# Kernel optimization log

Hardware: AMD Instinct MI355X
Metric: run time of the kernel (lower is better)

The kernel has to match this reference:

```python
import jax, jax.numpy as jnp
import numpy as np

B, S, D = 2, 2048, 1024
FFN = 4096
E, TOPK = 4, 2
H, WIN = 8, 128
EPS = 1e-6


def rmsnorm(x, w):
    rms = jax.lax.rsqrt(jnp.mean(x * x, axis=-1, keepdims=True) + EPS)
    return x * rms * w


def linear_scan(x, a):
    """h_t = a_t * h_{t-1} + x_t along axis=1, via associative scan."""
    def comb(c1, c2):
        a1, x1 = c1
        a2, x2 = c2
        return (a1 * a2, a2 * x1 + x2)
    _, h = jax.lax.associative_scan(comb, (a, x), axis=1)
    return h


def mingru_expert(xn, Wg, bg, Wv, bv, Wd, bd):
    g = xn @ Wg + bg
    v = xn @ Wv + bv
    d = xn @ Wd + bd
    x_scan = jax.nn.sigmoid(g) * jnp.tanh(v)
    a = 0.001 + 0.998 * jax.nn.sigmoid(d)
    return linear_scan(x_scan, a)


def setup_inputs() -> dict:
    key = jax.random.key(0)
    ks = jax.random.split(key, 16)
    sc = 0.02
    return {
        "x": jax.random.normal(ks[0], (B, S, D), jnp.float32),
        "rms_mix_w": jnp.ones((D,), jnp.float32),
        "gate_w": jax.random.normal(ks[1], (D, E), jnp.float32) * sc,
        "Wg": jax.random.normal(ks[2], (E, D, D), jnp.float32) * sc,
        "bg": jnp.zeros((E, D), jnp.float32),
        "Wv": jax.random.normal(ks[3], (E, D, D), jnp.float32) * sc,
        "bv": jnp.zeros((E, D), jnp.float32),
        "Wd": jax.random.normal(ks[4], (E, D, D), jnp.float32) * sc,
        "bd": jnp.ones((E, D), jnp.float32),  # decay_bias_init = 1.0
        "rms_attn_w": jnp.ones((D,), jnp.float32),
        "w_qkv": jax.random.normal(ks[5], (D, 3 * D), jnp.float32) * sc,
        "w_attn_out": jax.random.normal(ks[6], (D, D), jnp.float32) * sc,
        "rms_ffn_w": jnp.ones((D,), jnp.float32),
        "w_ffn_gate": jax.random.normal(ks[7], (D, FFN), jnp.float32) * sc,
        "w_ffn_up": jax.random.normal(ks[8], (D, FFN), jnp.float32) * sc,
        "w_ffn_out": jax.random.normal(ks[9], (FFN, D), jnp.float32) * sc,
    }


def reference(x, rms_mix_w, gate_w, Wg, bg, Wv, bv, Wd, bd,
              rms_attn_w, w_qkv, w_attn_out,
              rms_ffn_w, w_ffn_gate, w_ffn_up, w_ffn_out):
    # --- MoE-MinGRU mixer -------------------------------------------------
    xn = rmsnorm(x, rms_mix_w)
    gate_logits = xn @ gate_w                         # [B,S,E]
    top_vals, top_idx = jax.lax.top_k(gate_logits, TOPK)
    weights = jax.nn.softmax(top_vals, axis=-1)       # [B,S,K]
    expert_outs = jax.vmap(mingru_expert, in_axes=(None, 0, 0, 0, 0, 0, 0))(
        xn, Wg, bg, Wv, bv, Wd, bd)                   # [E,B,S,D]
    expert_outs = jnp.moveaxis(expert_outs, 0, 2)     # [B,S,E,D]
    gathered = jnp.take_along_axis(expert_outs, top_idx[..., None], axis=2)  # [B,S,K,D]
    mix = jnp.sum(weights[..., None] * gathered, axis=2)
    x = x + mix

    # --- Sliding-window causal attention ----------------------------------
    xn = rmsnorm(x, rms_attn_w)
    dh = D // H
    qkv = (xn @ w_qkv).reshape(B, S, 3, H, dh)
    q, k, v = qkv[:, :, 0], qkv[:, :, 1], qkv[:, :, 2]  # [B,S,H,dh]
    scores = jnp.einsum("bqhd,bkhd->bhqk", q, k) / jnp.sqrt(jnp.float32(dh))
    i = jnp.arange(S)[:, None]
    j = jnp.arange(S)[None, :]
    allowed = (j <= i) & (j > i - WIN)
    scores = jnp.where(allowed, scores, -jnp.inf)
    attn = jax.nn.softmax(scores, axis=-1)
    ao = jnp.einsum("bhqk,bkhd->bqhd", attn, v).reshape(B, S, D)
    x = x + ao @ w_attn_out

    # --- SwiGLU FFN --------------------------------------------------------
    xn = rmsnorm(x, rms_ffn_w)
    ffn = (jax.nn.silu(xn @ w_ffn_gate) * (xn @ w_ffn_up)) @ w_ffn_out
    return x + ffn
```

## Files before the change

kernel.cpp:

```cpp
#include <hip/hip_runtime.h>
#include <hip/hip_bf16.h>
#include <math.h>

constexpr int kB   = 2;
constexpr int kS   = 2048;
constexpr int kD   = 1024;
constexpr int kFFN = 4096;
constexpr int kM   = kB * kS;
constexpr int kH   = 8;
constexpr int kDH  = 128;
constexpr int kNC  = 64;
constexpr int kT   = kS / kNC;
constexpr int kNE  = 12288;

typedef unsigned short u16;
typedef __attribute__((ext_vector_type(8))) short short8;
typedef __attribute__((ext_vector_type(4))) float f32x4;

__device__ __forceinline__ float sigf(float x) { return 1.0f / (1.0f + __expf(-x)); }
__device__ __forceinline__ float bu2f(u16 u) { return __uint_as_float(((unsigned)u) << 16); }
__device__ __forceinline__ u16 f2bu(float f) {
    __hip_bfloat16 h = __float2bfloat16(f);
    return reinterpret_cast<u16&>(h);
}
__device__ __forceinline__ void async16(const void* g, void* l) {
    __builtin_amdgcn_global_load_lds((const __attribute__((address_space(1))) void*)g,
                                     (__attribute__((address_space(3))) void*)l, 16, 0, 0);
}
__device__ __forceinline__ int xcd_swz(int orig, int nwg) {
    const int xcd = orig & 7;
    const int q8 = nwg >> 3, r8 = nwg & 7;
    return (xcd < r8 ? xcd * (q8 + 1) : r8 * (q8 + 1) + (xcd - r8) * q8) + (orig >> 3);
}

__global__ __launch_bounds__(256) void rmsnorm_k(const float* __restrict__ x,
                                                 const float* __restrict__ w,
                                                 u16* __restrict__ o)
{
    __shared__ float red[4];
    const int row = blockIdx.x;
    const int t = threadIdx.x;
    float4 v = ((const float4*)(x + (size_t)row * kD))[t];
    float ss = v.x*v.x + v.y*v.y + v.z*v.z + v.w*v.w;
    #pragma unroll
    for (int m = 32; m; m >>= 1) ss += __shfl_xor(ss, m);
    if ((t & 63) == 0) red[t >> 6] = ss;
    __syncthreads();
    float tot = red[0] + red[1] + red[2] + red[3];
    float r = rsqrtf(tot * (1.0f / (float)kD) + 1e-6f);
    float4 wv = ((const float4*)w)[t];
    ushort4 u;
    u.x = f2bu(v.x * r * wv.x); u.y = f2bu(v.y * r * wv.y);
    u.z = f2bu(v.z * r * wv.z); u.w = f2bu(v.w * r * wv.w);
    ((ushort4*)(o + (size_t)row * kD))[t] = u;
}

__global__ __launch_bounds__(64) void routing_k(const float* __restrict__ x,
                                                const float* __restrict__ wmix,
                                                const float* __restrict__ gw,
                                                float* __restrict__ wts,
                                                int* __restrict__ idx)
{
    const int row = blockIdx.x;
    const int lane = threadIdx.x;
    const float* xr = x + (size_t)row * kD;
    float ss = 0.0f;
    for (int d = lane; d < kD; d += 64) { float v = xr[d]; ss = fmaf(v, v, ss); }
    #pragma unroll
    for (int m = 32; m; m >>= 1) ss += __shfl_xor(ss, m);
    float r = rsqrtf(ss * (1.0f / (float)kD) + 1e-6f);

    float a0 = 0, a1 = 0, a2 = 0, a3 = 0;
    for (int d = lane; d < kD; d += 64) {
        float xv = xr[d] * wmix[d];
        float4 g = ((const float4*)gw)[d];
        a0 = fmaf(xv, g.x, a0);
        a1 = fmaf(xv, g.y, a1);
        a2 = fmaf(xv, g.z, a2);
        a3 = fmaf(xv, g.w, a3);
    }
    #pragma unroll
    for (int m = 32; m; m >>= 1) {
        a0 += __shfl_xor(a0, m);
        a1 += __shfl_xor(a1, m);
        a2 += __shfl_xor(a2, m);
        a3 += __shfl_xor(a3, m);
    }
    if (lane == 0) {
        float a[4] = {a0, a1, a2, a3};
        int i0 = 0; float v0 = a[0];
        #pragma unroll
        for (int e = 1; e < 4; ++e) if (a[e] > v0) { v0 = a[e]; i0 = e; }
        int i1 = -1; float v1 = -INFINITY;
        #pragma unroll
        for (int e = 0; e < 4; ++e) if (e != i0 && a[e] > v1) { v1 = a[e]; i1 = e; }
        float e1 = __expf(r * (v1 - v0));
        float dn = 1.0f + e1;
        wts[row * 2 + 0] = 1.0f / dn;
        wts[row * 2 + 1] = e1 / dn;
        idx[row * 2 + 0] = i0;
        idx[row * 2 + 1] = i1;
    }
}

__global__ __launch_bounds__(256) void transp_k(const float* __restrict__ src,
                                                u16* __restrict__ dst,
                                                int rows, int cols,
                                                size_t sstride, size_t dstride)
{
    __shared__ float t[32][33];
    const float* s = src + blockIdx.z * sstride;
    u16* d = dst + blockIdx.z * dstride;
    const int c0 = blockIdx.x * 32, r0 = blockIdx.y * 32;
    const int tc = threadIdx.x & 31, tr4 = (threadIdx.x >> 5) * 4;
    #pragma unroll
    for (int i = 0; i < 4; ++i)
        t[tr4 + i][tc] = s[(size_t)(r0 + tr4 + i) * cols + c0 + tc];
    __syncthreads();
    #pragma unroll
    for (int i = 0; i < 4; ++i) {
        int cc = tr4 + i;
        d[(size_t)(c0 + cc) * rows + r0 + tc] = f2bu(t[tc][cc]);
    }
}

__global__ __launch_bounds__(256) void biaspack_k(const float* __restrict__ bg,
                                                  const float* __restrict__ bv,
                                                  const float* __restrict__ bd,
                                                  float* __restrict__ pb)
{
    int e = blockIdx.y;
    int r = blockIdx.x * 256 + threadIdx.x;
    const float* src = (r < 1024) ? bg : (r < 2048) ? bv : bd;
    pb[e * 3072 + r] = src[e * 1024 + (r & 1023)];
}

template<bool BIAS, bool SILU, bool MUL, bool NT>
__global__ __launch_bounds__(512, 2) void gemmA_k(
    const u16* __restrict__ A, const u16* __restrict__ BT,
    const float* __restrict__ bias, const u16* __restrict__ mulsrc,
    u16* __restrict__ Cout, int N, int K)
{
    __shared__ __align__(16) u16 lds[2][32768];
    const int tid = threadIdx.x;
    const int l = tid & 63;
    const int w = tid >> 6;
    const int wr = w >> 2, wc = w & 3;
    const int fr = l & 15, g = l >> 4;

    const int gx = gridDim.x;
    const int wg = xcd_swz(blockIdx.y * gx + blockIdx.x, gx * gridDim.y);
    const int bm = (wg / gx) * 256, bn = (wg % gx) * 256;

    const int srow = l >> 3;
    const int scol = (l & 7) ^ srow;
    const u16* gA = A  + (size_t)(bm + srow) * K + scol * 8;
    const u16* gB = BT + (size_t)(bn + srow) * K + scol * 8;

    auto STAGE = [&](int kt, int sb) {
        u16* dst = lds[sb] + l * 8;
        const int k0 = kt * 64;
        #pragma unroll
        for (int i = 0; i < 4; ++i) {
            int chunk = w * 4 + i;
            async16(gA + (size_t)chunk * 8 * K + k0, dst + chunk * 512);
            async16(gB + (size_t)chunk * 8 * K + k0, dst + 16384 + chunk * 512);
        }
    };

    f32x4 acc[8][4];
    #pragma unroll
    for (int m = 0; m < 8; ++m)
        #pragma unroll
        for (int n = 0; n < 4; ++n) acc[m][n] = (f32x4){0.f, 0.f, 0.f, 0.f};

    STAGE(0, 0);
    __syncthreads();
    const int nt = K >> 6;
    for (int t = 0; t < nt; ++t) {
        const int cb = t & 1;
        if (t + 1 < nt) STAGE(t + 1, cb ^ 1);
        const u16* bA = lds[cb];
        const u16* bB = lds[cb] + 16384;
        #pragma unroll
        for (int ks = 0; ks < 2; ++ks) {
            const int xo = ((ks * 4 + g) ^ (fr & 7)) * 8;
            short8 b[4];
            #pragma unroll
            for (int n = 0; n < 4; ++n)
                b[n] = *(const short8*)(bB + (wc * 64 + n * 16 + fr) * 64 + xo);
            #pragma unroll
            for (int m = 0; m < 8; ++m) {
                short8 a = *(const short8*)(bA + (wr * 128 + m * 16 + fr) * 64 + xo);
                #pragma unroll
                for (int n = 0; n < 4; ++n)
                    acc[m][n] = __builtin_amdgcn_mfma_f32_16x16x32_bf16(a, b[n], acc[m][n], 0, 0, 0);
            }
        }
        __syncthreads();
    }

    const int orow0 = bm + wr * 128 + g * 4;
    const int ocol0 = bn + wc * 64 + fr;
    float bi[4];
    if constexpr (BIAS) {
        #pragma unroll
        for (int n = 0; n < 4; ++n) bi[n] = bias[ocol0 + n * 16];
    }
    #pragma unroll
    for (int m = 0; m < 8; ++m) {
        #pragma unroll
        for (int r = 0; r < 4; ++r) {
            const size_t ro = (size_t)(orow0 + m * 16 + r) * N;
            #pragma unroll
            for (int n = 0; n < 4; ++n) {
                const size_t off = ro + ocol0 + n * 16;
                float v = acc[m][n][r];
                if constexpr (BIAS) v += bi[n];
                if constexpr (SILU) v = v * sigf(v);
                if constexpr (MUL)  v *= bu2f(mulsrc[off]);
                if constexpr (NT) __builtin_nontemporal_store((short)f2bu(v), (short*)(Cout + off));
                else              Cout[off] = f2bu(v);
            }
        }
    }
}

__global__ __launch_bounds__(512, 2) void gemmO_k(
    const u16* __restrict__ A, const u16* __restrict__ BT,
    const float* __restrict__ res, float* __restrict__ Cout,
    int N, int K)
{
    __shared__ __align__(16) u16 lds[2][20480];
    const int tid = threadIdx.x;
    const int l = tid & 63;
    const int w = tid >> 6;
    const int wr = w >> 1, wc = w & 1;
    const int fr = l & 15, g = l >> 4;

    const int gx = gridDim.x;
    const int wg = xcd_swz(blockIdx.y * gx + blockIdx.x, gx * gridDim.y);
    const int bm = (wg / gx) * 256, bn = (wg % gx) * 64;

    const int srow = l >> 3;
    const int scol = (l & 7) ^ srow;
    const u16* gA = A  + (size_t)(bm + srow) * K + scol * 8;
    const u16* gB = BT + (size_t)(bn + srow) * K + scol * 8;

    auto STAGE = [&](int kt, int sb) {
        u16* dst = lds[sb] + l * 8;
        const int k0 = kt * 64;
        #pragma unroll
        for (int i = 0; i < 4; ++i) {
            int chunk = w * 4 + i;
            async16(gA + (size_t)chunk * 8 * K + k0, dst + chunk * 512);
        }
        async16(gB + (size_t)w * 8 * K + k0, dst + 16384 + w * 512);
    };

    f32x4 acc[4][2];
    #pragma unroll
    for (int m = 0; m < 4; ++m)
        #pragma unroll
        for (int n = 0; n < 2; ++n) acc[m][n] = (f32x4){0.f, 0.f, 0.f, 0.f};

    STAGE(0, 0);
    __syncthreads();
    const int nt = K >> 6;
    for (int t = 0; t < nt; ++t) {
        const int cb = t & 1;
        if (t + 1 < nt) STAGE(t + 1, cb ^ 1);
        const u16* bA = lds[cb];
        const u16* bB = lds[cb] + 16384;
        #pragma unroll
        for (int ks = 0; ks < 2; ++ks) {
            const int xo = ((ks * 4 + g) ^ (fr & 7)) * 8;
            short8 a[4], b[2];
            #pragma unroll
            for (int m = 0; m < 4; ++m)
                a[m] = *(const short8*)(bA + (wr * 64 + m * 16 + fr) * 64 + xo);
            #pragma unroll
            for (int n = 0; n < 2; ++n)
                b[n] = *(const short8*)(bB + (wc * 32 + n * 16 + fr) * 64 + xo);
            #pragma unroll
            for (int m = 0; m < 4; ++m)
                #pragma unroll
                for (int n = 0; n < 2; ++n)
                    acc[m][n] = __builtin_amdgcn_mfma_f32_16x16x32_bf16(a[m], b[n], acc[m][n], 0, 0, 0);
        }
        __syncthreads();
    }

    const int orow0 = bm + wr * 64 + g * 4;
    const int ocol0 = bn + wc * 32 + fr;
    #pragma unroll
    for (int m = 0; m < 4; ++m) {
        #pragma unroll
        for (int r = 0; r < 4; ++r) {
            const size_t ro = (size_t)(orow0 + m * 16 + r) * N;
            #pragma unroll
            for (int n = 0; n < 2; ++n) {
                const size_t off = ro + ocol0 + n * 16;
                Cout[off] = acc[m][n][r] + res[off];
            }
        }
    }
}

__global__ __launch_bounds__(256) void scan1_k(const u16* __restrict__ gvdall,
                                               float* __restrict__ sumA,
                                               float* __restrict__ sumX)
{
    const int e = blockIdx.y;
    int i = blockIdx.x * 256 + threadIdx.x;
    int d = i & (kD - 1);
    int c = (i >> 10) & (kNC - 1);
    int b = i >> 16;
    const u16* gvd = gvdall + e * 3072;
    size_t base = ((size_t)b * kS + c * kT) * kNE + d;
    float A = 1.0f, X = 0.0f;
    for (int t = 0; t < kT; ++t) {
        size_t ix = base + (size_t)t * kNE;
        float xs = sigf(bu2f(gvd[ix])) * tanhf(bu2f(gvd[ix + 1024]));
        float a  = 0.001f + 0.998f * sigf(bu2f(gvd[ix + 2048]));
        A *= a;
        X = fmaf(a, X, xs);
    }
    size_t si = ((size_t)(e * kNC + c) * kB + b) * kD + d;
    sumA[si] = A;
    sumX[si] = X;
}

__global__ __launch_bounds__(256) void scan2_k(const float* __restrict__ sumA,
                                               const float* __restrict__ sumX,
                                               float* __restrict__ carry)
{
    const int e = blockIdx.y;
    int bd = blockIdx.x * 256 + threadIdx.x;
    float h = 0.0f;
    for (int c = 0; c < kNC; ++c) {
        size_t si = ((size_t)(e * kNC + c)) * (kB * kD) + bd;
        carry[si] = h;
        h = fmaf(sumA[si], h, sumX[si]);
    }
}

__global__ __launch_bounds__(256) void scan3_k(const u16* __restrict__ gvdall,
                                               const float* __restrict__ carry,
                                               const int* __restrict__ tidx,
                                               u16* __restrict__ slot0,
                                               u16* __restrict__ slot1)
{
    const int e = blockIdx.y;
    int i = blockIdx.x * 256 + threadIdx.x;
    int d = i & (kD - 1);
    int c = (i >> 10) & (kNC - 1);
    int b = i >> 16;
    const u16* gvd = gvdall + e * 3072;
    size_t base = ((size_t)b * kS + c * kT) * kNE + d;
    float h = carry[((size_t)(e * kNC + c) * kB + b) * kD + d];
    const int tok0 = b * kS + c * kT;
    for (int t = 0; t < kT; ++t) {
        size_t ix = base + (size_t)t * kNE;
        float xs = sigf(bu2f(gvd[ix])) * tanhf(bu2f(gvd[ix + 1024]));
        float a  = 0.001f + 0.998f * sigf(bu2f(gvd[ix + 2048]));
        h = fmaf(a, h, xs);
        const int tok = tok0 + t;
        const size_t o = (size_t)tok * kD + d;
        if (e == tidx[tok * 2])          slot0[o] = f2bu(h);
        else if (e == tidx[tok * 2 + 1]) slot1[o] = f2bu(h);
    }
}

__global__ __launch_bounds__(256) void mix_k(const float* __restrict__ x,
                                             const u16* __restrict__ slot0,
                                             const u16* __restrict__ slot1,
                                             const float* __restrict__ wts,
                                             float* __restrict__ xo)
{
    size_t i = (size_t)blockIdx.x * 256 + threadIdx.x;
    int m = (int)(i >> 8);
    float w0 = wts[m * 2 + 0], w1 = wts[m * 2 + 1];
    float4 xv = ((const float4*)x)[i];
    ushort4 h0 = ((const ushort4*)slot0)[i];
    ushort4 h1 = ((const ushort4*)slot1)[i];
    float4 o;
    o.x = xv.x + w0 * bu2f(h0.x) + w1 * bu2f(h1.x);
    o.y = xv.y + w0 * bu2f(h0.y) + w1 * bu2f(h1.y);
    o.z = xv.z + w0 * bu2f(h0.z) + w1 * bu2f(h1.z);
    o.w = xv.w + w0 * bu2f(h0.w) + w1 * bu2f(h1.w);
    ((float4*)xo)[i] = o;
}

__global__ __launch_bounds__(256) void transpV_k(const u16* __restrict__ qkvb,
                                                 u16* __restrict__ vT)
{
    __shared__ u16 t[64][68];
    const int tid = threadIdx.x;
    const int s0 = blockIdx.x * 64;
    const int d0 = blockIdx.y * 64;
    const int bh = blockIdx.z;
    const int bb = bh >> 3, hh = bh & 7;
    const u16* src = qkvb + (size_t)(bb * kS + s0) * 3072 + 2048 + hh * kDH + d0;
    for (int idx = tid; idx < 64 * 16; idx += 256) {
        int sl = idx >> 4, c4 = (idx & 15) * 4;
        *(ushort4*)&t[sl][c4] = *(const ushort4*)(src + (size_t)sl * 3072 + c4);
    }
    __syncthreads();
    u16* dst = vT + ((size_t)bh * kDH + d0) * kS + s0;
    for (int idx = tid; idx < 64 * 16; idx += 256) {
        int dl = idx >> 4, s4 = (idx & 15) * 4;
        ushort4 v;
        v.x = t[s4 + 0][dl]; v.y = t[s4 + 1][dl];
        v.z = t[s4 + 2][dl]; v.w = t[s4 + 3][dl];
        *(ushort4*)(dst + (size_t)dl * kS + s4) = v;
    }
}

__global__ __launch_bounds__(256) void attn_mfma_k(const u16* __restrict__ qkvb,
                                                   const u16* __restrict__ vT,
                                                   u16* __restrict__ aob)
{
    __shared__ __align__(16) u16 KV[26112];
    __shared__ __align__(16) u16 P[4 * 16 * 200];

    const int tid = threadIdx.x;
    const int lane = tid & 63;
    const int w = tid >> 6;
    const int fr = lane & 15, g = lane >> 4;
    const int q0 = blockIdx.x * 64;
    const int hh = blockIdx.y;
    const int bb = blockIdx.z;
    const int kbase = q0 - 128;
    const float scale = 0.08838834764831845f;

    const u16* qkv_b = qkvb + (size_t)bb * kS * 3072 + hh * kDH;

    for (int idx = tid; idx < 192 * 16; idx += 256) {
        int k = idx >> 4, c = idx & 15;
        int kg = kbase + k; if (kg < 0) kg = 0;
        short8 v = *(const short8*)(qkv_b + (size_t)kg * 3072 + 1024 + c * 8);
        *(short8*)(&KV[k * 136 + c * 8]) = v;
    }
    short8 qf[4];
    {
        const u16* qrow = qkv_b + (size_t)(q0 + w * 16 + fr) * 3072 + g * 8;
        #pragma unroll
        for (int s = 0; s < 4; ++s) qf[s] = *(const short8*)(qrow + s * 32);
    }
    __syncthreads();

    f32x4 sacc[12];
    #pragma unroll
    for (int f = 0; f < 12; ++f) sacc[f] = (f32x4){0.f, 0.f, 0.f, 0.f};
    #pragma unroll
    for (int s = 0; s < 4; ++s) {
        #pragma unroll
        for (int f = 0; f < 12; ++f) {
            short8 bfr = *(const short8*)(&KV[(f * 16 + fr) * 136 + s * 32 + g * 8]);
            sacc[f] = __builtin_amdgcn_mfma_f32_16x16x32_bf16(qf[s], bfr, sacc[f], 0, 0, 0);
        }
    }

    float p[12][4];
    #pragma unroll
    for (int r = 0; r < 4; ++r) {
        const int ql = w * 16 + g * 4 + r;
        int kmin = 128 - q0; if (kmin < ql + 1) kmin = ql + 1;
        const int kmax = ql + 128;
        float mx = -1e30f;
        #pragma unroll
        for (int f = 0; f < 12; ++f) {
            int kl = f * 16 + fr;
            float sv = (kl >= kmin && kl <= kmax) ? sacc[f][r] * scale : -1e30f;
            p[f][r] = sv;
            mx = fmaxf(mx, sv);
        }
        mx = fmaxf(mx, __shfl_xor(mx, 1));
        mx = fmaxf(mx, __shfl_xor(mx, 2));
        mx = fmaxf(mx, __shfl_xor(mx, 4));
        mx = fmaxf(mx, __shfl_xor(mx, 8));
        float l = 0.f;
        #pragma unroll
        for (int f = 0; f < 12; ++f) { float e = __expf(p[f][r] - mx); p[f][r] = e; l += e; }
        l += __shfl_xor(l, 1);
        l += __shfl_xor(l, 2);
        l += __shfl_xor(l, 4);
        l += __shfl_xor(l, 8);
        float linv = 1.0f / l;
        #pragma unroll
        for (int f = 0; f < 12; ++f) p[f][r] *= linv;
    }

    {
        u16* pw = &P[(w * 16) * 200];
        #pragma unroll
        for (int r = 0; r < 4; ++r)
            #pragma unroll
            for (int f = 0; f < 12; ++f)
                pw[(g * 4 + r) * 200 + f * 16 + fr] = f2bu(p[f][r]);
    }
    __syncthreads();

    {
        const u16* vrow = vT + (size_t)(bb * kH + hh) * kDH * kS;
        for (int idx = tid; idx < 128 * 25; idx += 256) {
            int d = idx / 25, c = idx % 25;
            if (c < 24) {
                int s0k = kbase + c * 8;
                short8 v;
                if (s0k < 0) v = (short8){0, 0, 0, 0, 0, 0, 0, 0};
                else v = *(const short8*)(vrow + (size_t)d * kS + s0k);
                *(short8*)(&KV[d * 200 + c * 8]) = v;
            }
        }
    }
    __syncthreads();

    f32x4 oacc[8];
    #pragma unroll
    for (int f = 0; f < 8; ++f) oacc[f] = (f32x4){0.f, 0.f, 0.f, 0.f};
    const u16* pr = &P[(w * 16 + fr) * 200 + g * 8];
    #pragma unroll
    for (int s = 0; s < 6; ++s) {
        short8 afr = *(const short8*)(pr + s * 32);
        #pragma unroll
        for (int f = 0; f < 8; ++f) {
            short8 bfr = *(const short8*)(&KV[(f * 16 + fr) * 200 + s * 32 + g * 8]);
            oacc[f] = __builtin_amdgcn_mfma_f32_16x16x32_bf16(afr, bfr, oacc[f], 0, 0, 0);
        }
    }
    u16* orow = aob + ((size_t)(bb * kS + q0 + w * 16 + g * 4) * kD) + hh * kDH + fr;
    #pragma unroll
    for (int r = 0; r < 4; ++r)
        #pragma unroll
        for (int f = 0; f < 8; ++f)
            orow[(size_t)r * kD + f * 16] = f2bu(oacc[f][r]);
}

extern "C" void kernel_launch(void* const* d_in, const int* in_sizes, int n_in,
                              void* d_out, int out_size, void* d_ws, size_t ws_size,
                              hipStream_t stream)
{
    (void)in_sizes; (void)n_in; (void)out_size; (void)ws_size;

    const float* x          = (const float*)d_in[0];
    const float* rms_mix    = (const float*)d_in[1];
    const float* gate_w     = (const float*)d_in[2];
    const float* Wg         = (const float*)d_in[3];
    const float* bg         = (const float*)d_in[4];
    const float* Wv         = (const float*)d_in[5];
    const float* bv         = (const float*)d_in[6];
    const float* Wd         = (const float*)d_in[7];
    const float* bd         = (const float*)d_in[8];
    const float* rms_attn   = (const float*)d_in[9];
    const float* w_qkv      = (const float*)d_in[10];
    const float* w_attn_out = (const float*)d_in[11];
    const float* rms_ffn    = (const float*)d_in[12];
    const float* w_ffn_gate = (const float*)d_in[13];
    const float* w_ffn_up   = (const float*)d_in[14];
    const float* w_ffn_out  = (const float*)d_in[15];
    float* out = (float*)d_out;

    const size_t MD = (size_t)kM * kD;
    const size_t M1 = 1024ull * 1024;
    char* p = (char*)d_ws;
    auto take = [&](size_t n) { char* r = p; p += (n + 255) & ~(size_t)255; return r; };

    u16*   xnb    = (u16*)take(MD * 2);
    u16*   gvdall = (u16*)take((size_t)kM * kNE * 2);
    u16*   qkvb   = gvdall;
    u16*   hidA   = gvdall;
    u16*   hidB   = gvdall + (size_t)kM * kFFN;
    u16*   ehb    = (u16*)take(4 * MD * 2);
    u16*   slot0  = ehb;
    u16*   slot1  = ehb + MD;
    u16*   aob    = ehb;
    u16*   vTb    = ehb + MD;
    u16*   wbuf   = (u16*)take(12ull * M1 * 2);
    float* pbias  = (float*)take((size_t)kNE * 4);
    float* sumA   = (float*)take(4ull * kNC * kB * kD * 4);
    float* sumX   = (float*)take(4ull * kNC * kB * kD * 4);
    float* carry  = (float*)take(4ull * kNC * kB * kD * 4);
    float* wts    = (float*)take((size_t)2 * kM * 4);
    int*   tidx   = (int*)take((size_t)2 * kM * 4);

    const dim3 blk(256);

    transp_k<<<dim3(32, 32, 4), blk, 0, stream>>>(Wg, wbuf, 1024, 1024,
                                                  (size_t)kD * kD, 3 * M1);
    transp_k<<<dim3(32, 32, 4), blk, 0, stream>>>(Wv, wbuf + M1, 1024, 1024,
                                                  (size_t)kD * kD, 3 * M1);
    transp_k<<<dim3(32, 32, 4), blk, 0, stream>>>(Wd, wbuf + 2 * M1, 1024, 1024,
                                                  (size_t)kD * kD, 3 * M1);
    biaspack_k<<<dim3(12, 4), blk, 0, stream>>>(bg, bv, bd, pbias);

    rmsnorm_k<<<kM, blk, 0, stream>>>(x, rms_mix, xnb);
    routing_k<<<kM, dim3(64), 0, stream>>>(x, rms_mix, gate_w, wts, tidx);

    gemmA_k<true, false, false, true><<<dim3(kNE / 256, kM / 256), dim3(512), 0, stream>>>(
        xnb, wbuf, pbias, nullptr, gvdall, kNE, 1024);
    const int scan_blocks = kB * kD * kNC / 256;
    scan1_k<<<dim3(scan_blocks, 4), blk, 0, stream>>>(gvdall, sumA, sumX);
    scan2_k<<<dim3(kB * kD / 256, 4), blk, 0, stream>>>(sumA, sumX, carry);
    scan3_k<<<dim3(scan_blocks, 4), blk, 0, stream>>>(gvdall, carry, tidx, slot0, slot1);

    mix_k<<<(int)(MD / 1024), blk, 0, stream>>>(x, slot0, slot1, wts, out);

    rmsnorm_k<<<kM, blk, 0, stream>>>(out, rms_attn, xnb);
    transp_k<<<dim3(96, 32, 1), blk, 0, stream>>>(w_qkv, wbuf, 1024, 3072, 0, 0);
    gemmA_k<false, false, false, false><<<dim3(3072 / 256, kM / 256), dim3(512), 0, stream>>>(
        xnb, wbuf, nullptr, nullptr, qkvb, 3072, 1024);
    transpV_k<<<dim3(kS / 64, 2, kB * kH), blk, 0, stream>>>(qkvb, vTb);
    attn_mfma_k<<<dim3(kS / 64, kH, kB), blk, 0, stream>>>(qkvb, vTb, aob);
    transp_k<<<dim3(32, 32, 1), blk, 0, stream>>>(w_attn_out, wbuf + 3 * M1, 1024, 1024, 0, 0);
    gemmO_k<<<dim3(1024 / 64, kM / 256), dim3(512), 0, stream>>>(
        aob, wbuf + 3 * M1, out, out, 1024, 1024);

    rmsnorm_k<<<kM, blk, 0, stream>>>(out, rms_ffn, xnb);
    transp_k<<<dim3(128, 32, 1), blk, 0, stream>>>(w_ffn_gate, wbuf + 4 * M1, 1024, 4096, 0, 0);
    transp_k<<<dim3(128, 32, 1), blk, 0, stream>>>(w_ffn_up, wbuf + 8 * M1, 1024, 4096, 0, 0);
    transp_k<<<dim3(32, 128, 1), blk, 0, stream>>>(w_ffn_out, wbuf, 4096, 1024, 0, 0);
    gemmA_k<false, true, false, false><<<dim3(kFFN / 256, kM / 256), dim3(512), 0, stream>>>(
        xnb, wbuf + 4 * M1, nullptr, nullptr, hidA, kFFN, 1024);
    gemmA_k<false, false, true, false><<<dim3(kFFN / 256, kM / 256), dim3(512), 0, stream>>>(
        xnb, wbuf + 8 * M1, nullptr, hidA, hidB, kFFN, 1024);
    gemmO_k<<<dim3(1024 / 64, kM / 256), dim3(512), 0, stream>>>(
        hidB, wbuf, out, out, 1024, 4096);
}
```

Before: 484.5 us.

## Fuse MoE mix with attention RMSNorm and reorder GEMM tile mapping

```diff
diff --git a/kernel.cpp b/kernel.cpp
--- a/kernel.cpp
+++ b/kernel.cpp
@@ -135,7 +135,7 @@
     pb[e * 3072 + r] = src[e * 1024 + (r & 1023)];
 }
 
-template<bool BIAS, bool SILU, bool MUL, bool NT>
+template<bool BIAS, bool SILU, bool MUL>
 __global__ __launch_bounds__(512, 2) void gemmA_k(
     const u16* __restrict__ A, const u16* __restrict__ BT,
     const float* __restrict__ bias, const u16* __restrict__ mulsrc,
@@ -148,9 +148,9 @@
     const int wr = w >> 2, wc = w & 3;
     const int fr = l & 15, g = l >> 4;
 
-    const int gx = gridDim.x;
-    const int wg = xcd_swz(blockIdx.y * gx + blockIdx.x, gx * gridDim.y);
-    const int bm = (wg / gx) * 256, bn = (wg % gx) * 256;
+    const int my = gridDim.y;
+    const int wg = xcd_swz(blockIdx.y * gridDim.x + blockIdx.x, gridDim.x * my);
+    const int bm = (wg % my) * 256, bn = (wg / my) * 256;
 
     const int srow = l >> 3;
     const int scol = (l & 7) ^ srow;
@@ -219,8 +219,7 @@
                 if constexpr (BIAS) v += bi[n];
                 if constexpr (SILU) v = v * sigf(v);
                 if constexpr (MUL)  v *= bu2f(mulsrc[off]);
-                if constexpr (NT) __builtin_nontemporal_store((short)f2bu(v), (short*)(Cout + off));
-                else              Cout[off] = f2bu(v);
+                Cout[off] = f2bu(v);
             }
         }
     }
@@ -238,9 +237,9 @@
     const int wr = w >> 1, wc = w & 1;
     const int fr = l & 15, g = l >> 4;
 
-    const int gx = gridDim.x;
-    const int wg = xcd_swz(blockIdx.y * gx + blockIdx.x, gx * gridDim.y);
-    const int bm = (wg / gx) * 256, bn = (wg % gx) * 64;
+    const int my = gridDim.y;
+    const int wg = xcd_swz(blockIdx.y * gridDim.x + blockIdx.x, gridDim.x * my);
+    const int bm = (wg % my) * 256, bn = (wg / my) * 64;
 
     const int srow = l >> 3;
     const int scol = (l & 7) ^ srow;
@@ -372,15 +371,19 @@
     }
 }
 
-__global__ __launch_bounds__(256) void mix_k(const float* __restrict__ x,
-                                             const u16* __restrict__ slot0,
-                                             const u16* __restrict__ slot1,
-                                             const float* __restrict__ wts,
-                                             float* __restrict__ xo)
-{
-    size_t i = (size_t)blockIdx.x * 256 + threadIdx.x;
-    int m = (int)(i >> 8);
-    float w0 = wts[m * 2 + 0], w1 = wts[m * 2 + 1];
+__global__ __launch_bounds__(256) void mixrms_k(const float* __restrict__ x,
+                                                const u16* __restrict__ slot0,
+                                                const u16* __restrict__ slot1,
+                                                const float* __restrict__ wts,
+                                                const float* __restrict__ w,
+                                                float* __restrict__ xo,
+                                                u16* __restrict__ xn)
+{
+    __shared__ float red[4];
+    const int row = blockIdx.x;
+    const int t = threadIdx.x;
+    const size_t i = (size_t)row * 256 + t;
+    float w0 = wts[row * 2 + 0], w1 = wts[row * 2 + 1];
     float4 xv = ((const float4*)x)[i];
     ushort4 h0 = ((const ushort4*)slot0)[i];
     ushort4 h1 = ((const ushort4*)slot1)[i];
@@ -390,6 +393,19 @@
     o.z = xv.z + w0 * bu2f(h0.z) + w1 * bu2f(h1.z);
     o.w = xv.w + w0 * bu2f(h0.w) + w1 * bu2f(h1.w);
     ((float4*)xo)[i] = o;
+
+    float ss = o.x*o.x + o.y*o.y + o.z*o.z + o.w*o.w;
+    #pragma unroll
+    for (int m = 32; m; m >>= 1) ss += __shfl_xor(ss, m);
+    if ((t & 63) == 0) red[t >> 6] = ss;
+    __syncthreads();
+    float tot = red[0] + red[1] + red[2] + red[3];
+    float r = rsqrtf(tot * (1.0f / (float)kD) + 1e-6f);
+    float4 wv = ((const float4*)w)[t];
+    ushort4 u;
+    u.x = f2bu(o.x * r * wv.x); u.y = f2bu(o.y * r * wv.y);
+    u.z = f2bu(o.z * r * wv.z); u.w = f2bu(o.w * r * wv.w);
+    ((ushort4*)(xn + (size_t)row * kD))[t] = u;
 }
 
 __global__ __launch_bounds__(256) void transpV_k(const u16* __restrict__ qkvb,
@@ -598,18 +614,17 @@
     rmsnorm_k<<<kM, blk, 0, stream>>>(x, rms_mix, xnb);
     routing_k<<<kM, dim3(64), 0, stream>>>(x, rms_mix, gate_w, wts, tidx);
 
-    gemmA_k<true, false, false, true><<<dim3(kNE / 256, kM / 256), dim3(512), 0, stream>>>(
+    gemmA_k<true, false, false><<<dim3(kNE / 256, kM / 256), dim3(512), 0, stream>>>(
         xnb, wbuf, pbias, nullptr, gvdall, kNE, 1024);
     const int scan_blocks = kB * kD * kNC / 256;
     scan1_k<<<dim3(scan_blocks, 4), blk, 0, stream>>>(gvdall, sumA, sumX);
     scan2_k<<<dim3(kB * kD / 256, 4), blk, 0, stream>>>(sumA, sumX, carry);
     scan3_k<<<dim3(scan_blocks, 4), blk, 0, stream>>>(gvdall, carry, tidx, slot0, slot1);
 
-    mix_k<<<(int)(MD / 1024), blk, 0, stream>>>(x, slot0, slot1, wts, out);
-
-    rmsnorm_k<<<kM, blk, 0, stream>>>(out, rms_attn, xnb);
+    mixrms_k<<<kM, blk, 0, stream>>>(x, slot0, slot1, wts, rms_attn, out, xnb);
+
     transp_k<<<dim3(96, 32, 1), blk, 0, stream>>>(w_qkv, wbuf, 1024, 3072, 0, 0);
-    gemmA_k<false, false, false, false><<<dim3(3072 / 256, kM / 256), dim3(512), 0, stream>>>(
+    gemmA_k<false, false, false><<<dim3(3072 / 256, kM / 256), dim3(512), 0, stream>>>(
         xnb, wbuf, nullptr, nullptr, qkvb, 3072, 1024);
     transpV_k<<<dim3(kS / 64, 2, kB * kH), blk, 0, stream>>>(qkvb, vTb);
     attn_mfma_k<<<dim3(kS / 64, kH, kB), blk, 0, stream>>>(qkvb, vTb, aob);
@@ -621,9 +636,9 @@
     transp_k<<<dim3(128, 32, 1), blk, 0, stream>>>(w_ffn_gate, wbuf + 4 * M1, 1024, 4096, 0, 0);
     transp_k<<<dim3(128, 32, 1), blk, 0, stream>>>(w_ffn_up, wbuf + 8 * M1, 1024, 4096, 0, 0);
     transp_k<<<dim3(32, 128, 1), blk, 0, stream>>>(w_ffn_out, wbuf, 4096, 1024, 0, 0);
-    gemmA_k<false, true, false, false><<<dim3(kFFN / 256, kM / 256), dim3(512), 0, stream>>>(
+    gemmA_k<false, true, false><<<dim3(kFFN / 256, kM / 256), dim3(512), 0, stream>>>(
         xnb, wbuf + 4 * M1, nullptr, nullptr, hidA, kFFN, 1024);
-    gemmA_k<false, false, true, false><<<dim3(kFFN / 256, kM / 256), dim3(512), 0, stream>>>(
+    gemmA_k<false, false, true><<<dim3(kFFN / 256, kM / 256), dim3(512), 0, stream>>>(
         xnb, wbuf + 8 * M1, nullptr, hidA, hidB, kFFN, 1024);
     gemmO_k<<<dim3(1024 / 64, kM / 256), dim3(512), 0, stream>>>(
         hidB, wbuf, out, out, 1024, 4096);
```

Measured after the change: 482.4 us. About the same (-0.4%).
